# Performance work log

Measured on AMD Instinct MI355X. Metric: run time of the kernel, lower is better.

## Reference

```python
import jax, jax.numpy as jnp
import numpy as np

N_A, N_C, N_L = 50000, 10000, 10000
HID = 128


def _gatv2(x_src, x_dst, src, dst, ea, Wl, bl, Wr, br, We, att, bias, H):
    # GATv2Conv (PyG) bipartite, edge_dim=1, concat=False (mean over heads), eval mode (no dropout)
    C = bias.shape[0]
    n_dst = x_dst.shape[0]
    xl = (x_src @ Wl + bl).reshape(-1, H, C)      # [N_src, H, C]
    xr = (x_dst @ Wr + br).reshape(-1, H, C)      # [N_dst, H, C]
    e = jax.nn.leaky_relu(xl[src] + xr[dst] + (ea @ We).reshape(-1, H, C), 0.2)  # [E,H,C]
    logit = jnp.einsum('ehc,hc->eh', e, att)      # [E,H]
    m = jax.ops.segment_max(logit, dst, num_segments=n_dst)
    m = jax.lax.stop_gradient(jnp.where(jnp.isfinite(m), m, 0.0))
    ex = jnp.exp(logit - m[dst])
    denom = jax.ops.segment_sum(ex, dst, num_segments=n_dst)
    alpha = ex / (denom[dst] + 1e-16)             # segment softmax over incoming edges
    out = jax.ops.segment_sum(alpha[:, :, None] * xl[src], dst, num_segments=n_dst)
    return out.mean(axis=1) + bias                # concat=False -> head mean + bias


def setup_inputs() -> dict:
    key = jax.random.key(0)
    ks = iter(jax.random.split(key, 80))
    def rn(shape, s=1.0):
        return jax.random.normal(next(ks), shape, jnp.float32) * s
    inp = {}
    inp['x_asset'] = rn((N_A, 512))
    inp['x_creator'] = rn((N_C, 2))
    inp['x_licensee'] = rn((N_L, 1))
    # edges: (name, E, src_max, dst_max)
    edges = [('cb', 50000, N_A, N_C), ('lt', 100000, N_A, N_L), ('sim', 200000, N_A, N_A),
             ('fw', 100000, N_A, N_A), ('rcb', 50000, N_C, N_A), ('rlt', 100000, N_L, N_A)]
    for name, E, smax, dmax in edges:
        inp[f'{name}_src'] = jax.random.randint(next(ks), (E,), 0, smax, jnp.int32)
        inp[f'{name}_dst'] = jax.random.randint(next(ks), (E,), 0, dmax, jnp.int32)
        inp[f'ea_{name}'] = rn((E, 1))
    w = 0.05  # param scale
    inp['Wp_a'] = rn((512, HID), w); inp['bp_a'] = rn((HID,), w)
    inp['Wp_c'] = rn((2, HID), w);   inp['bp_c'] = rn((HID,), w)
    inp['Wp_l'] = rn((1, HID), w);   inp['bp_l'] = rn((HID,), w)
    # layer 1: heads=2, stacked over the 6 relations
    H1 = 2
    inp['Wl1'] = rn((6, HID, H1 * HID), w); inp['bl1'] = rn((6, H1 * HID), w)
    inp['Wr1'] = rn((6, HID, H1 * HID), w); inp['br1'] = rn((6, H1 * HID), w)
    inp['We1'] = rn((6, 1, H1 * HID), w)
    inp['att1'] = rn((6, H1, HID), w); inp['bias1'] = rn((6, HID), w)
    # layer 2: heads=1
    inp['Wl2'] = rn((6, HID, HID), w); inp['bl2'] = rn((6, HID), w)
    inp['Wr2'] = rn((6, HID, HID), w); inp['br2'] = rn((6, HID), w)
    inp['We2'] = rn((6, 1, HID), w)
    inp['att2'] = rn((6, 1, HID), w); inp['bias2'] = rn((6, HID), w)
    inp['Wc1'] = rn((HID, HID), w); inp['bc1'] = rn((HID,), w)
    inp['Wc2'] = rn((HID, 3), w);   inp['bc2'] = rn((3,), w)
    inp['query_asset_index'] = 123
    return inp


def reference(x_asset, x_creator, x_licensee, Wp_a, bp_a, Wp_c, bp_c, Wp_l, bp_l,
              Wl1, bl1, Wr1, br1, We1, att1, bias1,
              Wl2, bl2, Wr2, br2, We2, att2, bias2,
              Wc1, bc1, Wc2, bc2,
              ea_cb, ea_lt, ea_sim, ea_fw, ea_rcb, ea_rlt,
              cb_src, cb_dst, lt_src, lt_dst, sim_src, sim_dst,
              fw_src, fw_dst, rcb_src, rcb_dst, rlt_src, rlt_dst,
              query_asset_index):
    x = {'Asset': x_asset @ Wp_a + bp_a,
         'Creator': x_creator @ Wp_c + bp_c,
         'Licensee': x_licensee @ Wp_l + bp_l}
    rels = [('Asset', 'Creator', cb_src, cb_dst, ea_cb),
            ('Asset', 'Licensee', lt_src, lt_dst, ea_lt),
            ('Asset', 'Asset', sim_src, sim_dst, ea_sim),
            ('Asset', 'Asset', fw_src, fw_dst, ea_fw),
            ('Creator', 'Asset', rcb_src, rcb_dst, ea_rcb),
            ('Licensee', 'Asset', rlt_src, rlt_dst, ea_rlt)]

    def hetero_layer(x, Wl, bl, Wr, br, We, att, bias, H):
        out = {k: jnp.zeros((v.shape[0], HID), v.dtype) for k, v in x.items()}
        for i, (st, dt, s, d, ea) in enumerate(rels):  # HeteroConv aggr='sum'
            out[dt] = out[dt] + _gatv2(x[st], x[dt], s, d, ea,
                                       Wl[i], bl[i], Wr[i], br[i], We[i], att[i], bias[i], H)
        return out

    x = hetero_layer(x, Wl1, bl1, Wr1, br1, We1, att1, bias1, 2)
    x = {k: jax.nn.relu(v) for k, v in x.items()}  # eval: dropout is identity
    x = hetero_layer(x, Wl2, bl2, Wr2, br2, We2, att2, bias2, 1)
    x = {k: jax.nn.relu(v) for k, v in x.items()}
    a = x['Asset'][query_asset_index]
    return jax.nn.relu(a @ Wc1 + bc1) @ Wc2 + bc2
```

## Files before the change

kernel.cpp:

```cpp
#include <hip/hip_runtime.h>
#include <math.h>

#define FAMAX 64
#define FCMAX 32
#define FLMAX 32
#define PAMAX 256
#define PCMAX 64
#define PLMAX 64
#define N1MAX 512
#define N2MAX 128

struct Inputs {
  const float *x_asset, *x_creator, *x_licensee;
  const float *Wp_a,*bp_a,*Wp_c,*bp_c,*Wp_l,*bp_l;
  const float *Wl1,*bl1,*Wr1,*br1,*We1,*att1,*bias1;
  const float *Wl2,*bl2,*Wr2,*br2,*We2,*att2,*bias2;
  const float *Wc1,*bc1,*Wc2,*bc2;
};

struct Edges {
  const int *cb_s,*cb_d;  const float* ea_cb;  int Ecb;
  const int *lt_s,*lt_d;  const float* ea_lt;  int Elt;
  const int *sim_s,*sim_d;const float* ea_sim; int Esim;
  const int *fw_s,*fw_d;  const float* ea_fw;  int Efw;
  const int *rcb_s,*rcb_d;const float* ea_rcb; int Ercb;
  const int *rlt_s,*rlt_d;const float* ea_rlt; int Erlt;
};

struct WSP {
  int* cnt;
  int *dfA,*dfC,*dfL;
  int *pfA,*pfC,*pfL;
  int *fa,*fc,*fl;
  int *pa,*pc,*pl;
  int* l2rel; int* l2src; float* l2ea;
  int* l1rel; int* l1src; int* l1dslot; float* l1ea;
  float *h0a,*h0c,*h0l;
  float *xr1a,*xr1c,*xr1l;
  float* xl1e;
  float* logit1;
  float *x1a,*x1c,*x1l;
  float* xr2q;
  float* xl2e;
  float* logit2;
};

__device__ __forceinline__ float leaky(float x){ return x > 0.f ? x : 0.2f*x; }

__device__ __forceinline__ void claim(int* flag, int* cnt, int* list, int node, int cap){
  int old = atomicCAS(&flag[node], 0, 1);
  if (old == 0){
    int k = atomicAdd(cnt, 1);
    if (k < cap){ list[k] = node; atomicExch(&flag[node], k + 2); }
    else atomicExch(&flag[node], 0);
  }
}

__global__ void k1_scan_l2(Edges eg, const int* qptr, WSP w){
  int q = qptr[0];
  if (blockIdx.x==0 && threadIdx.x==0){
    claim(w.dfA, &w.cnt[1], w.fa, q, FAMAX);
    claim(w.pfA, &w.cnt[5], w.pa, q, PAMAX);
  }
  int total = eg.Esim + eg.Efw + eg.Ercb + eg.Erlt;
  for (int i = blockIdx.x*blockDim.x + threadIdx.x; i < total; i += gridDim.x*blockDim.x){
    int j = i, rel; const int *sp,*dp; const float* ep;
    if (j < eg.Esim){ rel=2; sp=eg.sim_s; dp=eg.sim_d; ep=eg.ea_sim; }
    else { j -= eg.Esim;
      if (j < eg.Efw){ rel=3; sp=eg.fw_s; dp=eg.fw_d; ep=eg.ea_fw; }
      else { j -= eg.Efw;
        if (j < eg.Ercb){ rel=4; sp=eg.rcb_s; dp=eg.rcb_d; ep=eg.ea_rcb; }
        else { j -= eg.Ercb; rel=5; sp=eg.rlt_s; dp=eg.rlt_d; ep=eg.ea_rlt; }
      }
    }
    if (dp[j] == q){
      int src = sp[j];
      int k = atomicAdd(&w.cnt[0], 1);
      if (k < N2MAX){ w.l2rel[k]=rel; w.l2src[k]=src; w.l2ea[k]=ep[j]; }
      if (rel <= 3){ claim(w.dfA,&w.cnt[1],w.fa,src,FAMAX); claim(w.pfA,&w.cnt[5],w.pa,src,PAMAX); }
      else if (rel == 4){ claim(w.dfC,&w.cnt[2],w.fc,src,FCMAX); claim(w.pfC,&w.cnt[6],w.pc,src,PCMAX); }
      else { claim(w.dfL,&w.cnt[3],w.fl,src,FLMAX); claim(w.pfL,&w.cnt[7],w.pl,src,PLMAX); }
    }
  }
}

__global__ void k2_scan_l1(Edges eg, WSP w){
  int total = eg.Ecb+eg.Elt+eg.Esim+eg.Efw+eg.Ercb+eg.Erlt;
  for (int i = blockIdx.x*blockDim.x + threadIdx.x; i < total; i += gridDim.x*blockDim.x){
    int j = i, rel; const int *sp,*dp; const float* ep; const int* flag;
    if (j < eg.Ecb){ rel=0; sp=eg.cb_s; dp=eg.cb_d; ep=eg.ea_cb; flag=w.dfC; }
    else { j -= eg.Ecb;
    if (j < eg.Elt){ rel=1; sp=eg.lt_s; dp=eg.lt_d; ep=eg.ea_lt; flag=w.dfL; }
    else { j -= eg.Elt;
    if (j < eg.Esim){ rel=2; sp=eg.sim_s; dp=eg.sim_d; ep=eg.ea_sim; flag=w.dfA; }
    else { j -= eg.Esim;
    if (j < eg.Efw){ rel=3; sp=eg.fw_s; dp=eg.fw_d; ep=eg.ea_fw; flag=w.dfA; }
    else { j -= eg.Efw;
    if (j < eg.Ercb){ rel=4; sp=eg.rcb_s; dp=eg.rcb_d; ep=eg.ea_rcb; flag=w.dfA; }
    else { j -= eg.Ercb; rel=5; sp=eg.rlt_s; dp=eg.rlt_d; ep=eg.ea_rlt; flag=w.dfA; }}}}}
    int f = flag[dp[j]];
    if (f >= 2){
      int src = sp[j];
      int k = atomicAdd(&w.cnt[4], 1);
      if (k < N1MAX){ w.l1rel[k]=rel; w.l1src[k]=src; w.l1dslot[k]=f-2; w.l1ea[k]=ep[j]; }
      if (rel <= 3) claim(w.pfA,&w.cnt[5],w.pa,src,PAMAX);
      else if (rel == 4) claim(w.pfC,&w.cnt[6],w.pc,src,PCMAX);
      else claim(w.pfL,&w.cnt[7],w.pl,src,PLMAX);
    }
  }
}

__global__ void k3a_proj(Inputs in, WSP w){
  int b = blockIdx.x, t = threadIdx.x;
  if (b < PAMAX){
    __shared__ float xs[512];
    __shared__ float part[512];
    int npa = w.cnt[5] < PAMAX ? w.cnt[5] : PAMAX;
    if (b >= npa) return;
    int node = w.pa[b];
    xs[t] = in.x_asset[(size_t)node*512 + t];
    __syncthreads();
    int j = t & 127, g = t >> 7;
    float acc = 0.f;
    const float* W = in.Wp_a + (size_t)g*128*128 + j;
    const float* xg = xs + g*128;
    for (int k=0;k<128;k++) acc = fmaf(xg[k], W[(size_t)k*128], acc);
    part[t] = acc;
    __syncthreads();
    if (t < 128)
      w.h0a[(size_t)b*128 + t] = in.bp_a[t] + part[t] + part[128+t] + part[256+t] + part[384+t];
  } else if (b == PAMAX){
    int npc = w.cnt[6] < PCMAX ? w.cnt[6] : PCMAX;
    int j = t & 127, s0 = t >> 7;
    for (int s = s0; s < npc; s += 4){
      int node = w.pc[s];
      w.h0c[s*128 + j] = in.bp_c[j] + in.x_creator[node*2]*in.Wp_c[j]
                       + in.x_creator[node*2+1]*in.Wp_c[128+j];
    }
  } else {
    int npl = w.cnt[7] < PLMAX ? w.cnt[7] : PLMAX;
    int j = t & 127, s0 = t >> 7;
    for (int s = s0; s < npl; s += 4){
      int node = w.pl[s];
      w.h0l[s*128 + j] = in.bp_l[j] + in.x_licensee[node]*in.Wp_l[j];
    }
  }
}

__global__ void k3b_xr1(Inputs in, WSP w){
  __shared__ float h0[128];
  int b = blockIdx.x, t = threadIdx.x;
  int rel; const float* hsrc; float* dst;
  if (b < FAMAX*4){
    int slot = b >> 2, ridx = b & 3;
    int nfa = w.cnt[1] < FAMAX ? w.cnt[1] : FAMAX;
    if (slot >= nfa) return;
    rel = 2 + ridx;
    int ps = w.pfA[w.fa[slot]] - 2; if (ps < 0) return;
    hsrc = w.h0a + (size_t)ps*128;
    dst = w.xr1a + ((size_t)slot*4 + ridx)*256;
  } else if (b < FAMAX*4 + FCMAX){
    int slot = b - FAMAX*4;
    int nfc = w.cnt[2] < FCMAX ? w.cnt[2] : FCMAX;
    if (slot >= nfc) return;
    rel = 0;
    int ps = w.pfC[w.fc[slot]] - 2; if (ps < 0) return;
    hsrc = w.h0c + (size_t)ps*128;
    dst = w.xr1c + (size_t)slot*256;
  } else {
    int slot = b - FAMAX*4 - FCMAX;
    int nfl = w.cnt[3] < FLMAX ? w.cnt[3] : FLMAX;
    if (slot >= nfl) return;
    rel = 1;
    int ps = w.pfL[w.fl[slot]] - 2; if (ps < 0) return;
    hsrc = w.h0l + (size_t)ps*128;
    dst = w.xr1l + (size_t)slot*256;
  }
  if (t < 128) h0[t] = hsrc[t];
  __syncthreads();
  float acc = in.br1[rel*256 + t];
  const float* W = in.Wr1 + (size_t)rel*128*256 + t;
  for (int c=0;c<128;c++) acc = fmaf(h0[c], W[(size_t)c*256], acc);
  dst[t] = acc;
}

__global__ void k3c_edge(Inputs in, WSP w){
  __shared__ float h0[128];
  __shared__ float red[256];
  int i = blockIdx.x, t = threadIdx.x;
  int n1 = w.cnt[4] < N1MAX ? w.cnt[4] : N1MAX;
  if (i >= n1) return;
  int rel = w.l1rel[i], src = w.l1src[i], dslot = w.l1dslot[i];
  float ea = w.l1ea[i];
  int ps; const float* hsrc;
  if (rel <= 3){ ps = w.pfA[src]-2; hsrc = w.h0a + (size_t)(ps>0?ps:0)*128; }
  else if (rel == 4){ ps = w.pfC[src]-2; hsrc = w.h0c + (size_t)(ps>0?ps:0)*128; }
  else { ps = w.pfL[src]-2; hsrc = w.h0l + (size_t)(ps>0?ps:0)*128; }
  if (ps < 0){
    w.xl1e[(size_t)i*256 + t] = 0.f;
    if (t < 2) w.logit1[i*2 + t] = -INFINITY;
    return;
  }
  if (t < 128) h0[t] = hsrc[t];
  __syncthreads();
  float acc = in.bl1[rel*256 + t];
  const float* W = in.Wl1 + (size_t)rel*128*256 + t;
  for (int c=0;c<128;c++) acc = fmaf(h0[c], W[(size_t)c*256], acc);
  w.xl1e[(size_t)i*256 + t] = acc;
  const float* xr;
  if (rel >= 2) xr = w.xr1a + ((size_t)dslot*4 + (rel-2))*256;
  else if (rel == 0) xr = w.xr1c + (size_t)dslot*256;
  else xr = w.xr1l + (size_t)dslot*256;
  int h = t >> 7, c = t & 127;
  float e = leaky(acc + xr[t] + ea*in.We1[rel*256 + t]);
  red[t] = e * in.att1[(rel*2 + h)*128 + c];
  __syncthreads();
  for (int s=64; s>0; s>>=1){ if (c < s) red[t] += red[t+s]; __syncthreads(); }
  if (c == 0) w.logit1[i*2 + h] = red[t];
}

__global__ void k4_agg(Inputs in, WSP w){
  int b = blockIdx.x, j = threadIdx.x;
  int nfa = w.cnt[1] < FAMAX ? w.cnt[1] : FAMAX;
  int nfc = w.cnt[2] < FCMAX ? w.cnt[2] : FCMAX;
  int nfl = w.cnt[3] < FLMAX ? w.cnt[3] : FLMAX;
  int type, slot;
  if (b < FAMAX){ slot=b; if (slot>=nfa) return; type=0; }
  else if (b < FAMAX+FCMAX){ slot=b-FAMAX; if (slot>=nfc) return; type=1; }
  else { slot=b-FAMAX-FCMAX; if (slot>=nfl) return; type=2; }
  int n1 = w.cnt[4] < N1MAX ? w.cnt[4] : N1MAX;
  float out = 0.f;
  int r0, r1;
  if (type==0){ r0=2; r1=5; } else if (type==1){ r0=0; r1=0; } else { r0=1; r1=1; }
  for (int r=r0; r<=r1; r++){
    out += in.bias1[r*128 + j];
    float m0=-INFINITY, m1=-INFINITY;
    for (int i=0;i<n1;i++){
      if (w.l1rel[i]==r && w.l1dslot[i]==slot){
        m0 = fmaxf(m0, w.logit1[i*2]);
        m1 = fmaxf(m1, w.logit1[i*2+1]);
      }
    }
    if (m0 == -INFINITY) continue;
    float d0=0.f, d1=0.f, a0=0.f, a1=0.f;
    for (int i=0;i<n1;i++){
      if (w.l1rel[i]==r && w.l1dslot[i]==slot){
        float e0 = expf(w.logit1[i*2]   - m0);
        float e1 = expf(w.logit1[i*2+1] - m1);
        d0 += e0; d1 += e1;
        a0 = fmaf(e0, w.xl1e[(size_t)i*256 + j],       a0);
        a1 = fmaf(e1, w.xl1e[(size_t)i*256 + 128 + j], a1);
      }
    }
    out += 0.5f*(a0/(d0+1e-16f) + a1/(d1+1e-16f));
  }
  float v = fmaxf(out, 0.f);
  if (type==0) w.x1a[slot*128 + j] = v;
  else if (type==1) w.x1c[slot*128 + j] = v;
  else w.x1l[slot*128 + j] = v;
}

__global__ void k5a_xr2(Inputs in, WSP w, const int* qptr){
  __shared__ float xq[128];
  int t = threadIdx.x;
  int q = qptr[0];
  int qs = w.dfA[q] - 2;
  if (t < 128) xq[t] = w.x1a[(size_t)qs*128 + t];
  __syncthreads();
  int ridx = t >> 7, j = t & 127;
  int r = 2 + ridx;
  float acc = in.br2[r*128 + j];
  const float* W = in.Wr2 + (size_t)r*128*128 + j;
  for (int c=0;c<128;c++) acc = fmaf(xq[c], W[(size_t)c*128], acc);
  w.xr2q[ridx*128 + j] = acc;
}

__global__ void k5b_l2edge(Inputs in, WSP w){
  __shared__ float xs[128];
  __shared__ float red[128];
  int i = blockIdx.x, j = threadIdx.x;
  int n2 = w.cnt[0] < N2MAX ? w.cnt[0] : N2MAX;
  if (i >= n2) return;
  int rel = w.l2rel[i], src = w.l2src[i];
  float ea = w.l2ea[i];
  int f; const float* xb;
  if (rel <= 3){ f = w.dfA[src]; xb = w.x1a; }
  else if (rel == 4){ f = w.dfC[src]; xb = w.x1c; }
  else { f = w.dfL[src]; xb = w.x1l; }
  if (f < 2){
    w.xl2e[(size_t)i*128 + j] = 0.f;
    if (j == 0) w.logit2[i] = -INFINITY;
    return;
  }
  xs[j] = xb[(size_t)(f-2)*128 + j];
  __syncthreads();
  float acc = in.bl2[rel*128 + j];
  const float* W = in.Wl2 + (size_t)rel*128*128 + j;
  for (int c=0;c<128;c++) acc = fmaf(xs[c], W[(size_t)c*128], acc);
  w.xl2e[(size_t)i*128 + j] = acc;
  float e = leaky(acc + w.xr2q[(rel-2)*128 + j] + ea*in.We2[rel*128 + j]);
  red[j] = e * in.att2[rel*128 + j];
  __syncthreads();
  for (int s=64; s>0; s>>=1){ if (j < s) red[j] += red[j+s]; __syncthreads(); }
  if (j == 0) w.logit2[i] = red[0];
}

__global__ void k5c_final(Inputs in, WSP w, float* outp){
  __shared__ float x2[128];
  __shared__ float tt[128];
  int j = threadIdx.x;
  int n2 = w.cnt[0] < N2MAX ? w.cnt[0] : N2MAX;
  float o = 0.f;
  for (int r=2; r<=5; r++){
    o += in.bias2[r*128 + j];
    float m = -INFINITY;
    for (int i=0;i<n2;i++) if (w.l2rel[i]==r) m = fmaxf(m, w.logit2[i]);
    if (m == -INFINITY) continue;
    float d = 0.f, acc = 0.f;
    for (int i=0;i<n2;i++) if (w.l2rel[i]==r){
      float e = expf(w.logit2[i] - m);
      d += e;
      acc = fmaf(e, w.xl2e[(size_t)i*128 + j], acc);
    }
    o += acc/(d + 1e-16f);
  }
  x2[j] = fmaxf(o, 0.f);
  __syncthreads();
  float acc = in.bc1[j];
  for (int c=0;c<128;c++) acc = fmaf(x2[c], in.Wc1[c*128 + j], acc);
  tt[j] = fmaxf(acc, 0.f);
  __syncthreads();
  if (j < 3){
    float r = in.bc2[j];
    for (int c=0;c<128;c++) r = fmaf(tt[c], in.Wc2[c*3 + j], r);
    outp[j] = r;
  }
}

extern "C" void kernel_launch(void* const* d_in, const int* in_sizes, int n_in,
                              void* d_out, int out_size, void* d_ws, size_t ws_size,
                              hipStream_t stream){
  Inputs in;
  in.x_asset   = (const float*)d_in[0];
  in.x_creator = (const float*)d_in[1];
  in.x_licensee= (const float*)d_in[2];
  Edges eg;
  eg.cb_s =(const int*)d_in[3];  eg.cb_d =(const int*)d_in[4];  eg.ea_cb =(const float*)d_in[5];  eg.Ecb = in_sizes[3];
  eg.lt_s =(const int*)d_in[6];  eg.lt_d =(const int*)d_in[7];  eg.ea_lt =(const float*)d_in[8];  eg.Elt = in_sizes[6];
  eg.sim_s=(const int*)d_in[9];  eg.sim_d=(const int*)d_in[10]; eg.ea_sim=(const float*)d_in[11]; eg.Esim= in_sizes[9];
  eg.fw_s =(const int*)d_in[12]; eg.fw_d =(const int*)d_in[13]; eg.ea_fw =(const float*)d_in[14]; eg.Efw = in_sizes[12];
  eg.rcb_s=(const int*)d_in[15]; eg.rcb_d=(const int*)d_in[16]; eg.ea_rcb=(const float*)d_in[17]; eg.Ercb= in_sizes[15];
  eg.rlt_s=(const int*)d_in[18]; eg.rlt_d=(const int*)d_in[19]; eg.ea_rlt=(const float*)d_in[20]; eg.Erlt= in_sizes[18];
  in.Wp_a=(const float*)d_in[21]; in.bp_a=(const float*)d_in[22];
  in.Wp_c=(const float*)d_in[23]; in.bp_c=(const float*)d_in[24];
  in.Wp_l=(const float*)d_in[25]; in.bp_l=(const float*)d_in[26];
  in.Wl1=(const float*)d_in[27]; in.bl1=(const float*)d_in[28];
  in.Wr1=(const float*)d_in[29]; in.br1=(const float*)d_in[30];
  in.We1=(const float*)d_in[31]; in.att1=(const float*)d_in[32]; in.bias1=(const float*)d_in[33];
  in.Wl2=(const float*)d_in[34]; in.bl2=(const float*)d_in[35];
  in.Wr2=(const float*)d_in[36]; in.br2=(const float*)d_in[37];
  in.We2=(const float*)d_in[38]; in.att2=(const float*)d_in[39]; in.bias2=(const float*)d_in[40];
  in.Wc1=(const float*)d_in[41]; in.bc1=(const float*)d_in[42];
  in.Wc2=(const float*)d_in[43]; in.bc2=(const float*)d_in[44];
  const int* qptr = (const int*)d_in[45];

  char* p = (char*)d_ws;
  auto carve = [&](size_t n)->char*{ char* r = p; p += ((n + 255) & ~(size_t)255); return r; };
  WSP w;
  w.cnt  = (int*)carve(16*4);
  w.dfA  = (int*)carve(50000*4); w.dfC = (int*)carve(10000*4); w.dfL = (int*)carve(10000*4);
  w.pfA  = (int*)carve(50000*4); w.pfC = (int*)carve(10000*4); w.pfL = (int*)carve(10000*4);
  size_t zero_bytes = (size_t)(p - (char*)d_ws);
  w.fa = (int*)carve(FAMAX*4); w.fc = (int*)carve(FCMAX*4); w.fl = (int*)carve(FLMAX*4);
  w.pa = (int*)carve(PAMAX*4); w.pc = (int*)carve(PCMAX*4); w.pl = (int*)carve(PLMAX*4);
  w.l2rel=(int*)carve(N2MAX*4); w.l2src=(int*)carve(N2MAX*4); w.l2ea=(float*)carve(N2MAX*4);
  w.l1rel=(int*)carve(N1MAX*4); w.l1src=(int*)carve(N1MAX*4); w.l1dslot=(int*)carve(N1MAX*4); w.l1ea=(float*)carve(N1MAX*4);
  w.h0a=(float*)carve((size_t)PAMAX*128*4);
  w.h0c=(float*)carve((size_t)PCMAX*128*4);
  w.h0l=(float*)carve((size_t)PLMAX*128*4);
  w.xr1a=(float*)carve((size_t)FAMAX*4*256*4);
  w.xr1c=(float*)carve((size_t)FCMAX*256*4);
  w.xr1l=(float*)carve((size_t)FLMAX*256*4);
  w.xl1e=(float*)carve((size_t)N1MAX*256*4);
  w.logit1=(float*)carve((size_t)N1MAX*2*4);
  w.x1a=(float*)carve((size_t)FAMAX*128*4);
  w.x1c=(float*)carve((size_t)FCMAX*128*4);
  w.x1l=(float*)carve((size_t)FLMAX*128*4);
  w.xr2q=(float*)carve(4*128*4);
  w.xl2e=(float*)carve((size_t)N2MAX*128*4);
  w.logit2=(float*)carve(N2MAX*4);

  hipMemsetAsync(d_ws, 0, zero_bytes, stream);

  int tE2 = eg.Esim + eg.Efw + eg.Ercb + eg.Erlt;
  k1_scan_l2<<<(tE2+255)/256, 256, 0, stream>>>(eg, qptr, w);
  int tE1 = eg.Ecb + eg.Elt + tE2;
  k2_scan_l1<<<(tE1+255)/256, 256, 0, stream>>>(eg, w);
  k3a_proj<<<PAMAX+2, 512, 0, stream>>>(in, w);
  k3b_xr1<<<FAMAX*4 + FCMAX + FLMAX, 256, 0, stream>>>(in, w);
  k3c_edge<<<N1MAX, 256, 0, stream>>>(in, w);
  k4_agg<<<FAMAX + FCMAX + FLMAX, 128, 0, stream>>>(in, w);
  k5a_xr2<<<1, 512, 0, stream>>>(in, w, qptr);
  k5b_l2edge<<<N2MAX, 128, 0, stream>>>(in, w);
  k5c_final<<<1, 128, 0, stream>>>(in, w, (float*)d_out);
}
```

Baseline: 309.6 us.

## Fuse projection into per-node/edge GEMV kernels and merge layer-1 logits into aggregation

Drops the projected-node dedup lists (pfA/pa and related) and the separate projection kernel. Each destination-node block and each edge block now recomputes its own 512->128 input projection before the Wr1/Wl1 GEMV. The layer-1 attention logits move from the edge kernel into the aggregation kernel, and the layer-2 query xr2 projection is recomputed inside each edge block. Kernel launches go from six to three and the extra claim atomics disappear, at the cost of redundant projection work, notably a 512-wide projection per asset-source edge.

```diff
diff --git a/kernel.cpp b/kernel.cpp
--- a/kernel.cpp
+++ b/kernel.cpp
@@ -4,11 +4,9 @@
 #define FAMAX 64
 #define FCMAX 32
 #define FLMAX 32
-#define PAMAX 256
-#define PCMAX 64
-#define PLMAX 64
 #define N1MAX 512
 #define N2MAX 128
+#define DMAX  128
 
 struct Inputs {
   const float *x_asset, *x_creator, *x_licensee;
@@ -30,17 +28,12 @@
 struct WSP {
   int* cnt;
   int *dfA,*dfC,*dfL;
-  int *pfA,*pfC,*pfL;
   int *fa,*fc,*fl;
-  int *pa,*pc,*pl;
   int* l2rel; int* l2src; float* l2ea;
   int* l1rel; int* l1src; int* l1dslot; float* l1ea;
-  float *h0a,*h0c,*h0l;
   float *xr1a,*xr1c,*xr1l;
   float* xl1e;
-  float* logit1;
   float *x1a,*x1c,*x1l;
-  float* xr2q;
   float* xl2e;
   float* logit2;
 };
@@ -56,12 +49,35 @@
   }
 }
 
+__device__ __forceinline__ void proj256(int type, int node, const Inputs& in,
+                                        float* h0, float* xs, float* part){
+  int t = threadIdx.x;
+  if (type == 0){
+    xs[t]       = in.x_asset[(size_t)node*512 + t];
+    xs[t + 256] = in.x_asset[(size_t)node*512 + t + 256];
+    __syncthreads();
+    int j = t & 127, g2 = t >> 7;
+    float acc = 0.f;
+    const float* W = in.Wp_a + (size_t)g2*256*128 + j;
+    const float* xg = xs + g2*256;
+    for (int k=0;k<256;k++) acc = fmaf(xg[k], W[(size_t)k*128], acc);
+    part[t] = acc;
+    __syncthreads();
+    if (t < 128) h0[t] = in.bp_a[t] + part[t] + part[128 + t];
+  } else if (type == 1){
+    if (t < 128)
+      h0[t] = in.bp_c[t] + in.x_creator[node*2]*in.Wp_c[t]
+            + in.x_creator[node*2+1]*in.Wp_c[128+t];
+  } else {
+    if (t < 128)
+      h0[t] = in.bp_l[t] + in.x_licensee[node]*in.Wp_l[t];
+  }
+  __syncthreads();
+}
+
 __global__ void k1_scan_l2(Edges eg, const int* qptr, WSP w){
   int q = qptr[0];
-  if (blockIdx.x==0 && threadIdx.x==0){
-    claim(w.dfA, &w.cnt[1], w.fa, q, FAMAX);
-    claim(w.pfA, &w.cnt[5], w.pa, q, PAMAX);
-  }
+  if (blockIdx.x==0 && threadIdx.x==0) claim(w.dfA, &w.cnt[1], w.fa, q, FAMAX);
   int total = eg.Esim + eg.Efw + eg.Ercb + eg.Erlt;
   for (int i = blockIdx.x*blockDim.x + threadIdx.x; i < total; i += gridDim.x*blockDim.x){
     int j = i, rel; const int *sp,*dp; const float* ep;
@@ -77,9 +93,9 @@
       int src = sp[j];
       int k = atomicAdd(&w.cnt[0], 1);
       if (k < N2MAX){ w.l2rel[k]=rel; w.l2src[k]=src; w.l2ea[k]=ep[j]; }
-      if (rel <= 3){ claim(w.dfA,&w.cnt[1],w.fa,src,FAMAX); claim(w.pfA,&w.cnt[5],w.pa,src,PAMAX); }
-      else if (rel == 4){ claim(w.dfC,&w.cnt[2],w.fc,src,FCMAX); claim(w.pfC,&w.cnt[6],w.pc,src,PCMAX); }
-      else { claim(w.dfL,&w.cnt[3],w.fl,src,FLMAX); claim(w.pfL,&w.cnt[7],w.pl,src,PLMAX); }
+      if (rel <= 3) claim(w.dfA,&w.cnt[1],w.fa,src,FAMAX);
+      else if (rel == 4) claim(w.dfC,&w.cnt[2],w.fc,src,FCMAX);
+      else claim(w.dfL,&w.cnt[3],w.fl,src,FLMAX);
     }
   }
 }
@@ -100,127 +116,68 @@
     else { j -= eg.Ercb; rel=5; sp=eg.rlt_s; dp=eg.rlt_d; ep=eg.ea_rlt; flag=w.dfA; }}}}}
     int f = flag[dp[j]];
     if (f >= 2){
-      int src = sp[j];
       int k = atomicAdd(&w.cnt[4], 1);
-      if (k < N1MAX){ w.l1rel[k]=rel; w.l1src[k]=src; w.l1dslot[k]=f-2; w.l1ea[k]=ep[j]; }
-      if (rel <= 3) claim(w.pfA,&w.cnt[5],w.pa,src,PAMAX);
-      else if (rel == 4) claim(w.pfC,&w.cnt[6],w.pc,src,PCMAX);
-      else claim(w.pfL,&w.cnt[7],w.pl,src,PLMAX);
-    }
-  }
-}
-
-__global__ void k3a_proj(Inputs in, WSP w){
-  int b = blockIdx.x, t = threadIdx.x;
-  if (b < PAMAX){
-    __shared__ float xs[512];
-    __shared__ float part[512];
-    int npa = w.cnt[5] < PAMAX ? w.cnt[5] : PAMAX;
-    if (b >= npa) return;
-    int node = w.pa[b];
-    xs[t] = in.x_asset[(size_t)node*512 + t];
-    __syncthreads();
-    int j = t & 127, g = t >> 7;
-    float acc = 0.f;
-    const float* W = in.Wp_a + (size_t)g*128*128 + j;
-    const float* xg = xs + g*128;
-    for (int k=0;k<128;k++) acc = fmaf(xg[k], W[(size_t)k*128], acc);
-    part[t] = acc;
-    __syncthreads();
-    if (t < 128)
-      w.h0a[(size_t)b*128 + t] = in.bp_a[t] + part[t] + part[128+t] + part[256+t] + part[384+t];
-  } else if (b == PAMAX){
-    int npc = w.cnt[6] < PCMAX ? w.cnt[6] : PCMAX;
-    int j = t & 127, s0 = t >> 7;
-    for (int s = s0; s < npc; s += 4){
-      int node = w.pc[s];
-      w.h0c[s*128 + j] = in.bp_c[j] + in.x_creator[node*2]*in.Wp_c[j]
-                       + in.x_creator[node*2+1]*in.Wp_c[128+j];
-    }
-  } else {
-    int npl = w.cnt[7] < PLMAX ? w.cnt[7] : PLMAX;
-    int j = t & 127, s0 = t >> 7;
-    for (int s = s0; s < npl; s += 4){
-      int node = w.pl[s];
-      w.h0l[s*128 + j] = in.bp_l[j] + in.x_licensee[node]*in.Wp_l[j];
-    }
-  }
-}
-
-__global__ void k3b_xr1(Inputs in, WSP w){
+      if (k < N1MAX){ w.l1rel[k]=rel; w.l1src[k]=sp[j]; w.l1dslot[k]=f-2; w.l1ea[k]=ep[j]; }
+    }
+  }
+}
+
+__global__ void k3_fused(Inputs in, WSP w){
+  __shared__ float xs[512];
+  __shared__ float part[256];
   __shared__ float h0[128];
   int b = blockIdx.x, t = threadIdx.x;
-  int rel; const float* hsrc; float* dst;
-  if (b < FAMAX*4){
-    int slot = b >> 2, ridx = b & 3;
-    int nfa = w.cnt[1] < FAMAX ? w.cnt[1] : FAMAX;
-    if (slot >= nfa) return;
-    rel = 2 + ridx;
-    int ps = w.pfA[w.fa[slot]] - 2; if (ps < 0) return;
-    hsrc = w.h0a + (size_t)ps*128;
-    dst = w.xr1a + ((size_t)slot*4 + ridx)*256;
-  } else if (b < FAMAX*4 + FCMAX){
-    int slot = b - FAMAX*4;
-    int nfc = w.cnt[2] < FCMAX ? w.cnt[2] : FCMAX;
+  int nfa = w.cnt[1] < FAMAX ? w.cnt[1] : FAMAX;
+  int nfc = w.cnt[2] < FCMAX ? w.cnt[2] : FCMAX;
+  int nfl = w.cnt[3] < FLMAX ? w.cnt[3] : FLMAX;
+  if (b < FAMAX){
+    if (b >= nfa) return;
+    proj256(0, w.fa[b], in, h0, xs, part);
+    for (int ridx=0; ridx<4; ridx++){
+      int rel = 2 + ridx;
+      float acc = in.br1[rel*256 + t];
+      const float* W = in.Wr1 + (size_t)rel*128*256 + t;
+      for (int c=0;c<128;c++) acc = fmaf(h0[c], W[(size_t)c*256], acc);
+      w.xr1a[((size_t)b*4 + ridx)*256 + t] = acc;
+    }
+  } else if (b < FAMAX + FCMAX){
+    int slot = b - FAMAX;
     if (slot >= nfc) return;
-    rel = 0;
-    int ps = w.pfC[w.fc[slot]] - 2; if (ps < 0) return;
-    hsrc = w.h0c + (size_t)ps*128;
-    dst = w.xr1c + (size_t)slot*256;
+    proj256(1, w.fc[slot], in, h0, xs, part);
+    float acc = in.br1[0*256 + t];
+    const float* W = in.Wr1 + t;
+    for (int c=0;c<128;c++) acc = fmaf(h0[c], W[(size_t)c*256], acc);
+    w.xr1c[(size_t)slot*256 + t] = acc;
+  } else if (b < FAMAX + FCMAX + FLMAX){
+    int slot = b - FAMAX - FCMAX;
+    if (slot >= nfl) return;
+    proj256(2, w.fl[slot], in, h0, xs, part);
+    float acc = in.br1[1*256 + t];
+    const float* W = in.Wr1 + (size_t)1*128*256 + t;
+    for (int c=0;c<128;c++) acc = fmaf(h0[c], W[(size_t)c*256], acc);
+    w.xr1l[(size_t)slot*256 + t] = acc;
   } else {
-    int slot = b - FAMAX*4 - FCMAX;
-    int nfl = w.cnt[3] < FLMAX ? w.cnt[3] : FLMAX;
-    if (slot >= nfl) return;
-    rel = 1;
-    int ps = w.pfL[w.fl[slot]] - 2; if (ps < 0) return;
-    hsrc = w.h0l + (size_t)ps*128;
-    dst = w.xr1l + (size_t)slot*256;
-  }
-  if (t < 128) h0[t] = hsrc[t];
-  __syncthreads();
-  float acc = in.br1[rel*256 + t];
-  const float* W = in.Wr1 + (size_t)rel*128*256 + t;
-  for (int c=0;c<128;c++) acc = fmaf(h0[c], W[(size_t)c*256], acc);
-  dst[t] = acc;
-}
-
-__global__ void k3c_edge(Inputs in, WSP w){
-  __shared__ float h0[128];
+    int i = b - (FAMAX + FCMAX + FLMAX);
+    int n1 = w.cnt[4] < N1MAX ? w.cnt[4] : N1MAX;
+    if (i >= n1) return;
+    int rel = w.l1rel[i], src = w.l1src[i];
+    int stype = (rel <= 3) ? 0 : (rel == 4 ? 1 : 2);
+    proj256(stype, src, in, h0, xs, part);
+    float acc = in.bl1[rel*256 + t];
+    const float* W = in.Wl1 + (size_t)rel*128*256 + t;
+    for (int c=0;c<128;c++) acc = fmaf(h0[c], W[(size_t)c*256], acc);
+    w.xl1e[(size_t)i*256 + t] = acc;
+  }
+}
+
+__global__ void k4_agg(Inputs in, WSP w){
   __shared__ float red[256];
-  int i = blockIdx.x, t = threadIdx.x;
-  int n1 = w.cnt[4] < N1MAX ? w.cnt[4] : N1MAX;
-  if (i >= n1) return;
-  int rel = w.l1rel[i], src = w.l1src[i], dslot = w.l1dslot[i];
-  float ea = w.l1ea[i];
-  int ps; const float* hsrc;
-  if (rel <= 3){ ps = w.pfA[src]-2; hsrc = w.h0a + (size_t)(ps>0?ps:0)*128; }
-  else if (rel == 4){ ps = w.pfC[src]-2; hsrc = w.h0c + (size_t)(ps>0?ps:0)*128; }
-  else { ps = w.pfL[src]-2; hsrc = w.h0l + (size_t)(ps>0?ps:0)*128; }
-  if (ps < 0){
-    w.xl1e[(size_t)i*256 + t] = 0.f;
-    if (t < 2) w.logit1[i*2 + t] = -INFINITY;
-    return;
-  }
-  if (t < 128) h0[t] = hsrc[t];
-  __syncthreads();
-  float acc = in.bl1[rel*256 + t];
-  const float* W = in.Wl1 + (size_t)rel*128*256 + t;
-  for (int c=0;c<128;c++) acc = fmaf(h0[c], W[(size_t)c*256], acc);
-  w.xl1e[(size_t)i*256 + t] = acc;
-  const float* xr;
-  if (rel >= 2) xr = w.xr1a + ((size_t)dslot*4 + (rel-2))*256;
-  else if (rel == 0) xr = w.xr1c + (size_t)dslot*256;
-  else xr = w.xr1l + (size_t)dslot*256;
-  int h = t >> 7, c = t & 127;
-  float e = leaky(acc + xr[t] + ea*in.We1[rel*256 + t]);
-  red[t] = e * in.att1[(rel*2 + h)*128 + c];
-  __syncthreads();
-  for (int s=64; s>0; s>>=1){ if (c < s) red[t] += red[t+s]; __syncthreads(); }
-  if (c == 0) w.logit1[i*2 + h] = red[t];
-}
-
-__global__ void k4_agg(Inputs in, WSP w){
-  int b = blockIdx.x, j = threadIdx.x;
+  __shared__ int   lrel[N1MAX];
+  __shared__ int   lslot[N1MAX];
+  __shared__ float lea[N1MAX];
+  __shared__ float lg[DMAX][2];
+  __shared__ int   eid[DMAX];
+  int b = blockIdx.x, t = threadIdx.x;
   int nfa = w.cnt[1] < FAMAX ? w.cnt[1] : FAMAX;
   int nfc = w.cnt[2] < FCMAX ? w.cnt[2] : FCMAX;
   int nfl = w.cnt[3] < FLMAX ? w.cnt[3] : FLMAX;
@@ -229,54 +186,62 @@
   else if (b < FAMAX+FCMAX){ slot=b-FAMAX; if (slot>=nfc) return; type=1; }
   else { slot=b-FAMAX-FCMAX; if (slot>=nfl) return; type=2; }
   int n1 = w.cnt[4] < N1MAX ? w.cnt[4] : N1MAX;
+  for (int i = t; i < n1; i += 256){
+    lrel[i] = w.l1rel[i]; lslot[i] = w.l1dslot[i]; lea[i] = w.l1ea[i];
+  }
+  __syncthreads();
+  int h = t >> 7, c = t & 127;
   float out = 0.f;
   int r0, r1;
   if (type==0){ r0=2; r1=5; } else if (type==1){ r0=0; r1=0; } else { r0=1; r1=1; }
   for (int r=r0; r<=r1; r++){
-    out += in.bias1[r*128 + j];
+    if (t < 128) out += in.bias1[r*128 + t];
+    const float* xrp;
+    if (r >= 2) xrp = w.xr1a + ((size_t)slot*4 + (r-2))*256;
+    else if (r == 0) xrp = w.xr1c + (size_t)slot*256;
+    else xrp = w.xr1l + (size_t)slot*256;
+    float xrv = xrp[t];
+    float wev = in.We1[r*256 + t];
+    float atv = in.att1[(r*2 + h)*128 + c];
+    int nd = 0;
+    for (int i=0;i<n1 && nd<DMAX;i++){
+      if (lrel[i]==r && lslot[i]==slot){
+        float e = leaky(w.xl1e[(size_t)i*256 + t] + xrv + lea[i]*wev);
+        red[t] = e * atv;
+        __syncthreads();
+        for (int s=64; s>0; s>>=1){ if (c < s) red[t] += red[t+s]; __syncthreads(); }
+        if (t == 0){ lg[nd][0] = red[0]; lg[nd][1] = red[128]; eid[nd] = i; }
+        __syncthreads();
+        nd++;
+      }
+    }
+    if (nd == 0) continue;
     float m0=-INFINITY, m1=-INFINITY;
-    for (int i=0;i<n1;i++){
-      if (w.l1rel[i]==r && w.l1dslot[i]==slot){
-        m0 = fmaxf(m0, w.logit1[i*2]);
-        m1 = fmaxf(m1, w.logit1[i*2+1]);
+    for (int d=0; d<nd; d++){ m0 = fmaxf(m0, lg[d][0]); m1 = fmaxf(m1, lg[d][1]); }
+    float d0=0.f, d1=0.f;
+    for (int d=0; d<nd; d++){ d0 += expf(lg[d][0]-m0); d1 += expf(lg[d][1]-m1); }
+    if (t < 128){
+      float a0=0.f, a1=0.f;
+      for (int d=0; d<nd; d++){
+        int i = eid[d];
+        a0 = fmaf(expf(lg[d][0]-m0), w.xl1e[(size_t)i*256 + t],       a0);
+        a1 = fmaf(expf(lg[d][1]-m1), w.xl1e[(size_t)i*256 + 128 + t], a1);
       }
-    }
-    if (m0 == -INFINITY) continue;
-    float d0=0.f, d1=0.f, a0=0.f, a1=0.f;
-    for (int i=0;i<n1;i++){
-      if (w.l1rel[i]==r && w.l1dslot[i]==slot){
-        float e0 = expf(w.logit1[i*2]   - m0);
-        float e1 = expf(w.logit1[i*2+1] - m1);
-        d0 += e0; d1 += e1;
-        a0 = fmaf(e0, w.xl1e[(size_t)i*256 + j],       a0);
-        a1 = fmaf(e1, w.xl1e[(size_t)i*256 + 128 + j], a1);
-      }
-    }
-    out += 0.5f*(a0/(d0+1e-16f) + a1/(d1+1e-16f));
-  }
-  float v = fmaxf(out, 0.f);
-  if (type==0) w.x1a[slot*128 + j] = v;
-  else if (type==1) w.x1c[slot*128 + j] = v;
-  else w.x1l[slot*128 + j] = v;
-}
-
-__global__ void k5a_xr2(Inputs in, WSP w, const int* qptr){
+      out += 0.5f*(a0/(d0+1e-16f) + a1/(d1+1e-16f));
+    }
+    __syncthreads();
+  }
+  if (t < 128){
+    float v = fmaxf(out, 0.f);
+    if (type==0) w.x1a[slot*128 + t] = v;
+    else if (type==1) w.x1c[slot*128 + t] = v;
+    else w.x1l[slot*128 + t] = v;
+  }
+}
+
+__global__ void k5b_l2edge(Inputs in, WSP w, const int* qptr){
   __shared__ float xq[128];
-  int t = threadIdx.x;
-  int q = qptr[0];
-  int qs = w.dfA[q] - 2;
-  if (t < 128) xq[t] = w.x1a[(size_t)qs*128 + t];
-  __syncthreads();
-  int ridx = t >> 7, j = t & 127;
-  int r = 2 + ridx;
-  float acc = in.br2[r*128 + j];
-  const float* W = in.Wr2 + (size_t)r*128*128 + j;
-  for (int c=0;c<128;c++) acc = fmaf(xq[c], W[(size_t)c*128], acc);
-  w.xr2q[ridx*128 + j] = acc;
-}
-
-__global__ void k5b_l2edge(Inputs in, WSP w){
-  __shared__ float xs[128];
+  __shared__ float xsrc[128];
   __shared__ float red[128];
   int i = blockIdx.x, j = threadIdx.x;
   int n2 = w.cnt[0] < N2MAX ? w.cnt[0] : N2MAX;
@@ -292,13 +257,23 @@
     if (j == 0) w.logit2[i] = -INFINITY;
     return;
   }
-  xs[j] = xb[(size_t)(f-2)*128 + j];
-  __syncthreads();
-  float acc = in.bl2[rel*128 + j];
-  const float* W = in.Wl2 + (size_t)rel*128*128 + j;
-  for (int c=0;c<128;c++) acc = fmaf(xs[c], W[(size_t)c*128], acc);
-  w.xl2e[(size_t)i*128 + j] = acc;
-  float e = leaky(acc + w.xr2q[(rel-2)*128 + j] + ea*in.We2[rel*128 + j]);
+  int q = qptr[0];
+  int qs = w.dfA[q] - 2;
+  xq[j]   = w.x1a[(size_t)qs*128 + j];
+  xsrc[j] = xb[(size_t)(f-2)*128 + j];
+  __syncthreads();
+  float xr2 = in.br2[rel*128 + j];
+  {
+    const float* W = in.Wr2 + (size_t)rel*128*128 + j;
+    for (int c=0;c<128;c++) xr2 = fmaf(xq[c], W[(size_t)c*128], xr2);
+  }
+  float xl2 = in.bl2[rel*128 + j];
+  {
+    const float* W = in.Wl2 + (size_t)rel*128*128 + j;
+    for (int c=0;c<128;c++) xl2 = fmaf(xsrc[c], W[(size_t)c*128], xl2);
+  }
+  w.xl2e[(size_t)i*128 + j] = xl2;
+  float e = leaky(xl2 + xr2 + ea*in.We2[rel*128 + j]);
   red[j] = e * in.att2[rel*128 + j];
   __syncthreads();
   for (int s=64; s>0; s>>=1){ if (j < s) red[j] += red[j+s]; __syncthreads(); }
@@ -369,24 +344,17 @@
   WSP w;
   w.cnt  = (int*)carve(16*4);
   w.dfA  = (int*)carve(50000*4); w.dfC = (int*)carve(10000*4); w.dfL = (int*)carve(10000*4);
-  w.pfA  = (int*)carve(50000*4); w.pfC = (int*)carve(10000*4); w.pfL = (int*)carve(10000*4);
   size_t zero_bytes = (size_t)(p - (char*)d_ws);
   w.fa = (int*)carve(FAMAX*4); w.fc = (int*)carve(FCMAX*4); w.fl = (int*)carve(FLMAX*4);
-  w.pa = (int*)carve(PAMAX*4); w.pc = (int*)carve(PCMAX*4); w.pl = (int*)carve(PLMAX*4);
   w.l2rel=(int*)carve(N2MAX*4); w.l2src=(int*)carve(N2MAX*4); w.l2ea=(float*)carve(N2MAX*4);
   w.l1rel=(int*)carve(N1MAX*4); w.l1src=(int*)carve(N1MAX*4); w.l1dslot=(int*)carve(N1MAX*4); w.l1ea=(float*)carve(N1MAX*4);
-  w.h0a=(float*)carve((size_t)PAMAX*128*4);
-  w.h0c=(float*)carve((size_t)PCMAX*128*4);
-  w.h0l=(float*)carve((size_t)PLMAX*128*4);
   w.xr1a=(float*)carve((size_t)FAMAX*4*256*4);
   w.xr1c=(float*)carve((size_t)FCMAX*256*4);
   w.xr1l=(float*)carve((size_t)FLMAX*256*4);
   w.xl1e=(float*)carve((size_t)N1MAX*256*4);
-  w.logit1=(float*)carve((size_t)N1MAX*2*4);
   w.x1a=(float*)carve((size_t)FAMAX*128*4);
   w.x1c=(float*)carve((size_t)FCMAX*128*4);
   w.x1l=(float*)carve((size_t)FLMAX*128*4);
-  w.xr2q=(float*)carve(4*128*4);
   w.xl2e=(float*)carve((size_t)N2MAX*128*4);
   w.logit2=(float*)carve(N2MAX*4);
 
@@ -396,11 +364,8 @@
   k1_scan_l2<<<(tE2+255)/256, 256, 0, stream>>>(eg, qptr, w);
   int tE1 = eg.Ecb + eg.Elt + tE2;
   k2_scan_l1<<<(tE1+255)/256, 256, 0, stream>>>(eg, w);
-  k3a_proj<<<PAMAX+2, 512, 0, stream>>>(in, w);
-  k3b_xr1<<<FAMAX*4 + FCMAX + FLMAX, 256, 0, stream>>>(in, w);
-  k3c_edge<<<N1MAX, 256, 0, stream>>>(in, w);
-  k4_agg<<<FAMAX + FCMAX + FLMAX, 128, 0, stream>>>(in, w);
-  k5a_xr2<<<1, 512, 0, stream>>>(in, w, qptr);
-  k5b_l2edge<<<N2MAX, 128, 0, stream>>>(in, w);
+  k3_fused<<<FAMAX + FCMAX + FLMAX + N1MAX, 256, 0, stream>>>(in, w);
+  k4_agg<<<FAMAX + FCMAX + FLMAX, 256, 0, stream>>>(in, w);
+  k5b_l2edge<<<N2MAX, 128, 0, stream>>>(in, w, qptr);
   k5c_final<<<1, 128, 0, stream>>>(in, w, (float*)d_out);
 }
```

Result: no change. 315.3 us (+1.8%).
